# Performance work log

Measured on AMD Instinct MI355X. Metric: run time of the kernel, lower is better.

Reference implementation:

```python
import jax, jax.numpy as jnp
import numpy as np

C = 512
HEADS = 8
B, H, W = 2, 64, 64


def setup_inputs() -> dict:
    key = jax.random.key(0)
    k1, k2, k3, k4, k5 = jax.random.split(key, 5)
    s = 1.0 / np.sqrt(C)
    return {
        "hidden_states": jax.random.normal(k1, (B, C, H, W), dtype=jnp.float32),
        "qkv_w": jax.random.normal(k2, (3 * C, C), dtype=jnp.float32) * s,
        "qkv_b": jax.random.normal(k3, (3 * C,), dtype=jnp.float32) * 0.02,
        "proj_w": jax.random.normal(k4, (C, C), dtype=jnp.float32) * s,
        "proj_b": jax.random.normal(k5, (C,), dtype=jnp.float32) * 0.02,
    }


def reference(hidden_states, qkv_w, qkv_b, proj_w, proj_b):
    b, c, h, w = hidden_states.shape
    n = h * w  # sequence length
    heads = HEADS
    dim_head = c // heads
    scale = dim_head ** -0.5

    x = hidden_states.reshape(b, c, n)  # [b, c, n]
    # 1x1 conv1d == matmul over channel dim
    qkv = jnp.einsum("oc,bcn->bon", qkv_w, x) + qkv_b[None, :, None]  # [b, 3c, n]
    q, k, v = jnp.split(qkv, 3, axis=1)
    # [b, heads, dim_head, n] -> [b, heads, n, dim_head]
    def split_heads(t):
        return t.reshape(b, heads, dim_head, n).transpose(0, 1, 3, 2)
    q, k, v = split_heads(q), split_heads(k), split_heads(v)

    attn = jnp.einsum("bhqd,bhkd->bhqk", q, k) * scale  # [b, heads, n, n]
    attn = jax.nn.softmax(attn, axis=-1)
    out = jnp.einsum("bhqk,bhkd->bhqd", attn, v)  # [b, heads, n, dim_head]
    out = out.transpose(0, 1, 3, 2).reshape(b, c, n)  # [b, c, n]
    out = jnp.einsum("oc,bcn->bon", proj_w, out) + proj_b[None, :, None]
    return out  # [b, c, h*w] (matches torch module, no reshape back)
```

## Files before the change

kernel.cpp:

```cpp
#include <hip/hip_runtime.h>


#include <stdint.h>

typedef __attribute__((ext_vector_type(8))) short s16x8;
typedef __attribute__((ext_vector_type(4))) float f32x4;
typedef __attribute__((ext_vector_type(16))) float f32x16;
typedef __attribute__((ext_vector_type(4))) unsigned short u16x4;
typedef __attribute__((ext_vector_type(2))) unsigned u32x2;
typedef __attribute__((ext_vector_type(4))) unsigned u32x4;

__device__ __forceinline__ unsigned short f2bf(float f) {
  unsigned u = __builtin_bit_cast(unsigned, f);
  u += 0x7fffu + ((u >> 16) & 1u);
  return (unsigned short)(u >> 16);
}

__device__ __forceinline__ float bf2f(short s) {
  return __builtin_bit_cast(float, ((unsigned)(unsigned short)s) << 16);
}

__device__ __forceinline__ unsigned cvt_pk_bf16(float lo, float hi) {
  unsigned r;
  asm("v_cvt_pk_bf16_f32 %0, %1, %2" : "=v"(r) : "v"(lo), "v"(hi));
  return r;
}

__device__ __forceinline__ void gl_lds16(const void* g, void* l) {
  auto gp = reinterpret_cast<const __attribute__((address_space(1))) char*>(
      reinterpret_cast<uintptr_t>(g));
  auto lp = reinterpret_cast<__attribute__((address_space(3))) char*>(
      reinterpret_cast<uintptr_t>(l));
  __builtin_amdgcn_global_load_lds(gp, lp, 16, 0, 0);
}

__global__ __launch_bounds__(256) void prep_weights(
    const float* __restrict__ qkv_w, const float* __restrict__ proj_w,
    short* __restrict__ wq, short* __restrict__ wp) {
  int t = blockIdx.x * 256 + threadIdx.x;
  const int NQ = 1536 * 512 / 4;
  if (t < NQ) {
    float4 v = ((const float4*)qkv_w)[t];
    u16x4 o; o[0] = f2bf(v.x); o[1] = f2bf(v.y); o[2] = f2bf(v.z); o[3] = f2bf(v.w);
    ((u16x4*)wq)[t] = o;
  } else {
    int t2 = t - NQ;
    float4 v = ((const float4*)proj_w)[t2];
    u16x4 o; o[0] = f2bf(v.x); o[1] = f2bf(v.y); o[2] = f2bf(v.z); o[3] = f2bf(v.w);
    ((u16x4*)wp)[t2] = o;
  }
}

__global__ __launch_bounds__(256) void prep_transpose(
    const float* __restrict__ x, short* __restrict__ xt) {
  __shared__ short TL[64 * 72];
  const int b = blockIdx.z, c0 = blockIdx.y * 64, n0 = blockIdx.x * 64;
  const int t = threadIdx.x;
  const int cr = t >> 4, n4 = (t & 15) * 4;
#pragma unroll
  for (int i = 0; i < 4; i++) {
    int c = cr + i * 16;
    float4 v = *(const float4*)(x + ((size_t)(b * 512 + c0 + c)) * 4096 + n0 + n4);
    TL[(n4 + 0) * 72 + c] = (short)f2bf(v.x);
    TL[(n4 + 1) * 72 + c] = (short)f2bf(v.y);
    TL[(n4 + 2) * 72 + c] = (short)f2bf(v.z);
    TL[(n4 + 3) * 72 + c] = (short)f2bf(v.w);
  }
  __syncthreads();
  const int n = t >> 2;
#pragma unroll
  for (int s2 = 0; s2 < 2; s2++) {
    int s = (t & 3) * 2 + s2;
    s16x8 v = *(const s16x8*)&TL[n * 72 + s * 8];
    *(s16x8*)(xt + ((size_t)(b * 4096 + n0 + n)) * 512 + c0 + s * 8) = v;
  }
}

__global__ __launch_bounds__(256) void qkv_gemm(
    const short* __restrict__ wq, const short* __restrict__ xt,
    const float* __restrict__ qkv_b,
    short* __restrict__ qkbuf,
    short* __restrict__ vbuf) {
  __shared__ short Al[128 * 40];
  __shared__ short Bl[128 * 40];
  const int b = blockIdx.z;
  const int m0 = blockIdx.y * 128, n0 = blockIdx.x * 128;
  const bool swapped = (blockIdx.y < 8);
  const int t = threadIdx.x, lane = t & 63, wid = t >> 6;
  const int wr = wid >> 1, wc = wid & 1;
  const int srow = t >> 1, scol = (t & 1) * 16;
  const short* gA = wq + (size_t)(m0 + srow) * 512 + scol;
  const short* gB = xt + ((size_t)(b * 4096 + n0 + srow)) * 512 + scol;
  short* lA = &Al[srow * 40 + scol];
  short* lB = &Bl[srow * 40 + scol];
  const short* As = swapped ? Bl : Al;
  const short* Bs = swapped ? Al : Bl;
  f32x4 acc[4][4] = {};
  for (int ks = 0; ks < 16; ks++) {
    *(s16x8*)lA       = *(const s16x8*)(gA + ks * 32);
    *(s16x8*)(lA + 8) = *(const s16x8*)(gA + ks * 32 + 8);
    *(s16x8*)lB       = *(const s16x8*)(gB + ks * 32);
    *(s16x8*)(lB + 8) = *(const s16x8*)(gB + ks * 32 + 8);
    __syncthreads();
    s16x8 af[4], bf[4];
#pragma unroll
    for (int i = 0; i < 4; i++) {
      af[i] = *(const s16x8*)&As[(wr * 64 + i * 16 + (lane & 15)) * 40 + ((lane >> 4) << 3)];
      bf[i] = *(const s16x8*)&Bs[(wc * 64 + i * 16 + (lane & 15)) * 40 + ((lane >> 4) << 3)];
    }
#pragma unroll
    for (int i = 0; i < 4; i++)
#pragma unroll
      for (int j = 0; j < 4; j++)
        acc[i][j] = __builtin_amdgcn_mfma_f32_16x16x32_bf16(af[i], bf[j], acc[i][j], 0, 0, 0);
    __syncthreads();
  }
  if (!swapped) {
#pragma unroll
    for (int i = 0; i < 4; i++)
#pragma unroll
      for (int r = 0; r < 4; r++) {
        int orow = m0 + wr * 64 + i * 16 + ((lane >> 4) << 2) + r;
        float bias = qkv_b[orow];
#pragma unroll
        for (int j = 0; j < 4; j++) {
          int ncol = n0 + wc * 64 + j * 16 + (lane & 15);
          vbuf[((size_t)(b * 512 + orow - 1024)) * 4096 + ncol] = (short)f2bf(acc[i][j][r] + bias);
        }
      }
  } else {
    const float qs = (m0 < 512) ? 0.18033688f : 1.0f;
#pragma unroll
    for (int j = 0; j < 4; j++) {
      int ocol = m0 + wc * 64 + j * 16 + (lane & 15);
      float bias = qkv_b[ocol];
#pragma unroll
      for (int i = 0; i < 4; i++)
#pragma unroll
        for (int r = 0; r < 4; r++) {
          int nrow = n0 + wr * 64 + i * 16 + ((lane >> 4) << 2) + r;
          qkbuf[((size_t)(b * 4096 + nrow)) * 1024 + ocol] = (short)f2bf((acc[i][j][r] + bias) * qs);
        }
    }
  }
}

__global__ __launch_bounds__(256) void flash_attn(
    const short* __restrict__ qkbuf, const short* __restrict__ vbuf,
    short* __restrict__ opart,
    float* __restrict__ mlbuf) {
  __shared__ short Kl[2][64 * 64];
  __shared__ short Vl[2][64 * 64];
  const int t = threadIdx.x, lane = t & 63, wid = t >> 6;
  const int hi = lane >> 5, q32 = lane & 31;
  const int j = blockIdx.x;
  const int lid = ((j & 7) << 7) + (j >> 3);
  const int bh = lid >> 6, b = bh >> 3, h = bh & 7;
  const int rest = lid & 63;
  const int qc = rest >> 1, half = rest & 1;
  const int qb = qc * 128 + wid * 32;
  const int kt0 = half * 32;

  s16x8 qf[4];
  {
    const short* qrow = qkbuf + ((size_t)(b * 4096 + qb + q32)) * 1024 + h * 64 + hi * 8;
#pragma unroll
    for (int dc = 0; dc < 4; dc++) qf[dc] = *(const s16x8*)(qrow + dc * 16);
  }

  f32x16 oacc[2] = {};
  float m = -__builtin_inff();
  float l = 0.f;

  const int lrow = lane >> 3;
  const int lcolb = ((lane & 7) << 4) ^ (lrow << 4);
  const char* kp0 = (const char*)(qkbuf + ((size_t)(b * 4096 + kt0 * 64 + wid * 16 + lrow)) * 1024
                                  + 512 + h * 64) + lcolb;
  const char* kp1 = kp0 + 8 * 2048;
  const char* vp0 = (const char*)(vbuf + ((size_t)(b * 512 + h * 64 + wid * 16 + lrow)) * 4096
                                  + kt0 * 64) + lcolb;
  const char* vp1 = vp0 + 8 * 8192;

#define ISSUE_TILE(bi)                                                      \
  do {                                                                      \
    gl_lds16(kp0, &Kl[bi][(wid * 16 + 0) * 64]);                            \
    gl_lds16(kp1, &Kl[bi][(wid * 16 + 8) * 64]);                            \
    gl_lds16(vp0, &Vl[bi][(wid * 16 + 0) * 64]);                            \
    gl_lds16(vp1, &Vl[bi][(wid * 16 + 8) * 64]);                            \
    kp0 += 131072; kp1 += 131072; vp0 += 128; vp1 += 128;                   \
  } while (0)

  const int ksw = (q32 & 7) << 4;

  auto do_tile = [&](const short* Klb, const short* Vlb) {
#pragma unroll
    for (int kb = 0; kb < 2; kb++) {
      f32x16 st = {};
      const char* kr = (const char*)(Klb + (kb * 32 + q32) * 64);
      __builtin_amdgcn_s_setprio(1);
#pragma unroll
      for (int dc = 0; dc < 4; dc++) {
        s16x8 kf = *(const s16x8*)(kr + ((dc * 32 + hi * 16) ^ ksw));
        st = __builtin_amdgcn_mfma_f32_32x32x16_bf16(kf, qf[dc], st, 0, 0, 0);
      }
      __builtin_amdgcn_s_setprio(0);
      float x0 = fmaxf(st[0], st[1]),  x1 = fmaxf(st[2], st[3]);
      float x2 = fmaxf(st[4], st[5]),  x3 = fmaxf(st[6], st[7]);
      float x4 = fmaxf(st[8], st[9]),  x5 = fmaxf(st[10], st[11]);
      float x6 = fmaxf(st[12], st[13]), x7 = fmaxf(st[14], st[15]);
      x0 = fmaxf(x0, x1); x2 = fmaxf(x2, x3); x4 = fmaxf(x4, x5); x6 = fmaxf(x6, x7);
      x0 = fmaxf(x0, x2); x4 = fmaxf(x4, x6);
      float tm = fmaxf(x0, x4);
      tm = fmaxf(tm, __shfl_xor(tm, 32));
      if (!__all(tm <= m + 8.f)) {
        float mn = fmaxf(m, tm);
        float alpha = exp2f(m - mn);
        m = mn;
        l *= alpha;
#pragma unroll
        for (int di = 0; di < 2; di++)
#pragma unroll
          for (int r2 = 0; r2 < 16; r2++) oacc[di][r2] *= alpha;
      }
      float p[16];
      float ps = 0.f;
#pragma unroll
      for (int r2 = 0; r2 < 16; r2++) { p[r2] = exp2f(st[r2] - m); ps += p[r2]; }
      l += ps;
#pragma unroll
      for (int kh = 0; kh < 2; kh++) {
        unsigned A  = cvt_pk_bf16(p[kh * 8 + 0], p[kh * 8 + 1]);
        unsigned Bu = cvt_pk_bf16(p[kh * 8 + 4], p[kh * 8 + 5]);
        unsigned C  = cvt_pk_bf16(p[kh * 8 + 2], p[kh * 8 + 3]);
        unsigned D  = cvt_pk_bf16(p[kh * 8 + 6], p[kh * 8 + 7]);
        u32x2 r0 = __builtin_amdgcn_permlane32_swap(A, Bu, false, false);
        u32x2 r1 = __builtin_amdgcn_permlane32_swap(C, D, false, false);
        u32x4 uu; uu[0] = r0[0]; uu[1] = r1[0]; uu[2] = r0[1]; uu[3] = r1[1];
        s16x8 pf = __builtin_bit_cast(s16x8, uu);
        __builtin_amdgcn_s_setprio(1);
#pragma unroll
        for (int di = 0; di < 2; di++) {
          const char* vr = (const char*)(Vlb + (di * 32 + q32) * 64);
          s16x8 vf = *(const s16x8*)(vr + ((kb * 64 + kh * 32 + hi * 16) ^ ksw));
          oacc[di] = __builtin_amdgcn_mfma_f32_32x32x16_bf16(vf, pf, oacc[di], 0, 0, 0);
        }
        __builtin_amdgcn_s_setprio(0);
      }
    }
  };

  ISSUE_TILE(0);
#pragma unroll 1
  for (int it = 0; it < 16; it++) {
    __syncthreads();
    ISSUE_TILE(1);
    do_tile(Kl[0], Vl[0]);
    __syncthreads();
    if (it < 15) ISSUE_TILE(0);
    do_tile(Kl[1], Vl[1]);
  }
#undef ISSUE_TILE

  l += __shfl_xor(l, 32);
  const size_t prow = ((size_t)(half * 16 + bh) * 4096 + qb + q32) * 64;
#pragma unroll
  for (int di = 0; di < 2; di++)
#pragma unroll
    for (int blk = 0; blk < 4; blk++) {
      uint2 w;
      w.x = cvt_pk_bf16(oacc[di][blk * 4 + 0], oacc[di][blk * 4 + 1]);
      w.y = cvt_pk_bf16(oacc[di][blk * 4 + 2], oacc[di][blk * 4 + 3]);
      *(uint2*)(opart + prow + di * 32 + blk * 8 + hi * 4) = w;
    }
  if (hi == 0) {
    const size_t mrow = (size_t)(half * 16 + bh) * 4096 + qb + q32;
    ((float2*)mlbuf)[mrow] = make_float2(m, l);
  }
}

__global__ __launch_bounds__(256) void merge_halves(
    const short* __restrict__ opart, const float* __restrict__ mlbuf,
    short* __restrict__ aout) {
  const int row = blockIdx.x * 256 + threadIdx.x;
  const int bh = row >> 12, q = row & 4095, b = bh >> 3, h = bh & 7;
  float2 ml0 = ((const float2*)mlbuf)[row];
  float2 ml1 = ((const float2*)mlbuf)[65536 + row];
  float mm = fmaxf(ml0.x, ml1.x);
  float w0 = exp2f(ml0.x - mm), w1 = exp2f(ml1.x - mm);
  float inv = 1.f / (w0 * ml0.y + w1 * ml1.y);
  w0 *= inv; w1 *= inv;
  const s16x8* r0 = (const s16x8*)(opart + (size_t)row * 64);
  const s16x8* r1 = (const s16x8*)(opart + ((size_t)65536 + row) * 64);
  short* po = aout + ((size_t)(b * 4096 + q)) * 512 + h * 64;
#pragma unroll
  for (int sg = 0; sg < 8; sg++) {
    s16x8 a0 = r0[sg], a1 = r1[sg];
    float v[8];
#pragma unroll
    for (int i = 0; i < 8; i++) v[i] = w0 * bf2f(a0[i]) + w1 * bf2f(a1[i]);
    u32x4 uu;
#pragma unroll
    for (int k = 0; k < 4; k++) uu[k] = cvt_pk_bf16(v[2 * k], v[2 * k + 1]);
    *(s16x8*)(po + sg * 8) = __builtin_bit_cast(s16x8, uu);
  }
}

__global__ __launch_bounds__(256) void proj_gemm(
    const short* __restrict__ wp, const short* __restrict__ aout,
    const float* __restrict__ proj_b, float* __restrict__ out) {
  __shared__ short Al[128 * 40];
  __shared__ short Bl[128 * 40];
  const int b = blockIdx.z;
  const int m0 = blockIdx.y * 128, n0 = blockIdx.x * 128;
  const int t = threadIdx.x, lane = t & 63, wid = t >> 6;
  const int wr = wid >> 1, wc = wid & 1;
  const int srow = t >> 1, scol = (t & 1) * 16;
  const short* gA = wp + (size_t)(m0 + srow) * 512 + scol;
  const short* gB = aout + ((size_t)(b * 4096 + n0 + srow)) * 512 + scol;
  short* lA = &Al[srow * 40 + scol];
  short* lB = &Bl[srow * 40 + scol];
  f32x4 acc[4][4] = {};
  for (int ks = 0; ks < 16; ks++) {
    *(s16x8*)lA       = *(const s16x8*)(gA + ks * 32);
    *(s16x8*)(lA + 8) = *(const s16x8*)(gA + ks * 32 + 8);
    *(s16x8*)lB       = *(const s16x8*)(gB + ks * 32);
    *(s16x8*)(lB + 8) = *(const s16x8*)(gB + ks * 32 + 8);
    __syncthreads();
    s16x8 af[4], bf[4];
#pragma unroll
    for (int i = 0; i < 4; i++) {
      af[i] = *(const s16x8*)&Al[(wr * 64 + i * 16 + (lane & 15)) * 40 + ((lane >> 4) << 3)];
      bf[i] = *(const s16x8*)&Bl[(wc * 64 + i * 16 + (lane & 15)) * 40 + ((lane >> 4) << 3)];
    }
#pragma unroll
    for (int i = 0; i < 4; i++)
#pragma unroll
      for (int j = 0; j < 4; j++)
        acc[i][j] = __builtin_amdgcn_mfma_f32_16x16x32_bf16(af[i], bf[j], acc[i][j], 0, 0, 0);
    __syncthreads();
  }
#pragma unroll
  for (int i = 0; i < 4; i++)
#pragma unroll
    for (int r = 0; r < 4; r++) {
      int orow = m0 + wr * 64 + i * 16 + ((lane >> 4) << 2) + r;
      float bias = proj_b[orow];
#pragma unroll
      for (int j = 0; j < 4; j++) {
        int ncol = n0 + wc * 64 + j * 16 + (lane & 15);
        out[((size_t)(b * 512 + orow)) * 4096 + ncol] = acc[i][j][r] + bias;
      }
    }
}

extern "C" void kernel_launch(void* const* d_in, const int* in_sizes, int n_in,
                              void* d_out, int out_size, void* d_ws, size_t ws_size,
                              hipStream_t stream) {
  const float* x      = (const float*)d_in[0];
  const float* qkv_w  = (const float*)d_in[1];
  const float* qkv_b  = (const float*)d_in[2];
  const float* proj_w = (const float*)d_in[3];
  const float* proj_b = (const float*)d_in[4];
  float* out = (float*)d_out;
  char* ws = (char*)d_ws;
  short* wq = (short*)(ws);
  short* wp = (short*)(ws + 1572864);
  short* xt = (short*)(ws + 2097152);
  short* qk = (short*)(ws + 10485760);
  short* vb = (short*)(ws + 27262976);
  short* ao = (short*)(ws + 35651584);
  short* op = (short*)(ws + 44040192);
  float* ml = (float*)(ws + 60817408);

  prep_weights  <<<1024, 256, 0, stream>>>(qkv_w, proj_w, wq, wp);
  prep_transpose<<<dim3(64, 8, 2), 256, 0, stream>>>(x, xt);
  qkv_gemm      <<<dim3(32, 12, 2), 256, 0, stream>>>(wq, xt, qkv_b, qk, vb);
  flash_attn    <<<1024, 256, 0, stream>>>(qk, vb, op, ml);
  merge_halves  <<<256, 256, 0, stream>>>(op, ml, ao);
  proj_gemm     <<<dim3(32, 4, 2), 256, 0, stream>>>(wp, ao, proj_b, out);
}
```

Measured before the change: 254.9 us.

## Double-buffer QKV and proj GEMM tiles with direct global-to-LDS loads and swizzle

Both 1x1-conv GEMMs now use two LDS buffers per operand. Each buffer is filled with direct global-to-LDS loads (gl_lds16) for the next K step, issued right after the barrier so they overlap the current step's MFMAs, which removes one barrier per iteration. The padded 40-element row layout becomes an XOR-swizzled 32-element layout to avoid LDS bank conflicts without padding. MFMA sections are wrapped in s_setprio raises. The change relies on gl_lds16 being defined in the unseen part of the file and on its asynchronous completion being ordered correctly by the single barrier.

Result: faster. 240.0 us (-5.9%).

```diff
diff --git a/kernel.cpp b/kernel.cpp
--- a/kernel.cpp
+++ b/kernel.cpp
@@ -81,40 +81,57 @@
     const float* __restrict__ qkv_b,
     short* __restrict__ qkbuf,
     short* __restrict__ vbuf) {
-  __shared__ short Al[128 * 40];
-  __shared__ short Bl[128 * 40];
+  __shared__ short Al[2][128 * 32];
+  __shared__ short Bl[2][128 * 32];
   const int b = blockIdx.z;
   const int m0 = blockIdx.y * 128, n0 = blockIdx.x * 128;
   const bool swapped = (blockIdx.y < 8);
   const int t = threadIdx.x, lane = t & 63, wid = t >> 6;
   const int wr = wid >> 1, wc = wid & 1;
-  const int srow = t >> 1, scol = (t & 1) * 16;
-  const short* gA = wq + (size_t)(m0 + srow) * 512 + scol;
-  const short* gB = xt + ((size_t)(b * 4096 + n0 + srow)) * 512 + scol;
-  short* lA = &Al[srow * 40 + scol];
-  short* lB = &Bl[srow * 40 + scol];
-  const short* As = swapped ? Bl : Al;
-  const short* Bs = swapped ? Al : Bl;
+  const int rowoff = lane >> 2;
+  const int srcswz = (((lane & 3) ^ (rowoff & 3)) << 4);
+  const char* gA = (const char*)(wq + (size_t)(m0 + wid * 16 + rowoff) * 512) + srcswz;
+  const char* gB = (const char*)(xt + ((size_t)(b * 4096 + n0 + wid * 16 + rowoff)) * 512) + srcswz;
+  char* lA0 = (char*)&Al[0][0] + (wid * 16) * 64;
+  char* lA1 = (char*)&Al[1][0] + (wid * 16) * 64;
+  char* lB0 = (char*)&Bl[0][0] + (wid * 16) * 64;
+  char* lB1 = (char*)&Bl[1][0] + (wid * 16) * 64;
+
+#define GISSUE(bi, ks)                                                      \
+  do {                                                                      \
+    gl_lds16(gA + (ks) * 64,         (bi) ? lA1 : lA0);                     \
+    gl_lds16(gA + 65536 + (ks) * 64, ((bi) ? lA1 : lA0) + 64 * 64);         \
+    gl_lds16(gB + (ks) * 64,         (bi) ? lB1 : lB0);                     \
+    gl_lds16(gB + 65536 + (ks) * 64, ((bi) ? lB1 : lB0) + 64 * 64);         \
+  } while (0)
+
+  const int g4 = (lane >> 4) << 4;
+  const int rsw = (lane & 3) << 4;
   f32x4 acc[4][4] = {};
+
+  GISSUE(0, 0);
+#pragma unroll 1
   for (int ks = 0; ks < 16; ks++) {
-    *(s16x8*)lA       = *(const s16x8*)(gA + ks * 32);
-    *(s16x8*)(lA + 8) = *(const s16x8*)(gA + ks * 32 + 8);
-    *(s16x8*)lB       = *(const s16x8*)(gB + ks * 32);
-    *(s16x8*)(lB + 8) = *(const s16x8*)(gB + ks * 32 + 8);
     __syncthreads();
+    if (ks < 15) GISSUE((ks + 1) & 1, ks + 1);
+    const int bi = ks & 1;
+    const short* As = swapped ? Bl[bi] : Al[bi];
+    const short* Bs = swapped ? Al[bi] : Bl[bi];
     s16x8 af[4], bf[4];
 #pragma unroll
     for (int i = 0; i < 4; i++) {
-      af[i] = *(const s16x8*)&As[(wr * 64 + i * 16 + (lane & 15)) * 40 + ((lane >> 4) << 3)];
-      bf[i] = *(const s16x8*)&Bs[(wc * 64 + i * 16 + (lane & 15)) * 40 + ((lane >> 4) << 3)];
-    }
+      af[i] = *(const s16x8*)((const char*)As + (wr * 64 + i * 16 + (lane & 15)) * 64 + (g4 ^ rsw));
+      bf[i] = *(const s16x8*)((const char*)Bs + (wc * 64 + i * 16 + (lane & 15)) * 64 + (g4 ^ rsw));
+    }
+    __builtin_amdgcn_s_setprio(1);
 #pragma unroll
     for (int i = 0; i < 4; i++)
 #pragma unroll
       for (int j = 0; j < 4; j++)
         acc[i][j] = __builtin_amdgcn_mfma_f32_16x16x32_bf16(af[i], bf[j], acc[i][j], 0, 0, 0);
-    __syncthreads();
-  }
+    __builtin_amdgcn_s_setprio(0);
+  }
+#undef GISSUE
   if (!swapped) {
 #pragma unroll
     for (int i = 0; i < 4; i++)
@@ -308,37 +325,54 @@
 __global__ __launch_bounds__(256) void proj_gemm(
     const short* __restrict__ wp, const short* __restrict__ aout,
     const float* __restrict__ proj_b, float* __restrict__ out) {
-  __shared__ short Al[128 * 40];
-  __shared__ short Bl[128 * 40];
+  __shared__ short Al[2][128 * 32];
+  __shared__ short Bl[2][128 * 32];
   const int b = blockIdx.z;
   const int m0 = blockIdx.y * 128, n0 = blockIdx.x * 128;
   const int t = threadIdx.x, lane = t & 63, wid = t >> 6;
   const int wr = wid >> 1, wc = wid & 1;
-  const int srow = t >> 1, scol = (t & 1) * 16;
-  const short* gA = wp + (size_t)(m0 + srow) * 512 + scol;
-  const short* gB = aout + ((size_t)(b * 4096 + n0 + srow)) * 512 + scol;
-  short* lA = &Al[srow * 40 + scol];
-  short* lB = &Bl[srow * 40 + scol];
+  const int rowoff = lane >> 2;
+  const int srcswz = (((lane & 3) ^ (rowoff & 3)) << 4);
+  const char* gA = (const char*)(wp + (size_t)(m0 + wid * 16 + rowoff) * 512) + srcswz;
+  const char* gB = (const char*)(aout + ((size_t)(b * 4096 + n0 + wid * 16 + rowoff)) * 512) + srcswz;
+  char* lA0 = (char*)&Al[0][0] + (wid * 16) * 64;
+  char* lA1 = (char*)&Al[1][0] + (wid * 16) * 64;
+  char* lB0 = (char*)&Bl[0][0] + (wid * 16) * 64;
+  char* lB1 = (char*)&Bl[1][0] + (wid * 16) * 64;
+
+#define GISSUE(bi, ks)                                                      \
+  do {                                                                      \
+    gl_lds16(gA + (ks) * 64,         (bi) ? lA1 : lA0);                     \
+    gl_lds16(gA + 65536 + (ks) * 64, ((bi) ? lA1 : lA0) + 64 * 64);         \
+    gl_lds16(gB + (ks) * 64,         (bi) ? lB1 : lB0);                     \
+    gl_lds16(gB + 65536 + (ks) * 64, ((bi) ? lB1 : lB0) + 64 * 64);         \
+  } while (0)
+
+  const int g4 = (lane >> 4) << 4;
+  const int rsw = (lane & 3) << 4;
   f32x4 acc[4][4] = {};
+
+  GISSUE(0, 0);
+#pragma unroll 1
   for (int ks = 0; ks < 16; ks++) {
-    *(s16x8*)lA       = *(const s16x8*)(gA + ks * 32);
-    *(s16x8*)(lA + 8) = *(const s16x8*)(gA + ks * 32 + 8);
-    *(s16x8*)lB       = *(const s16x8*)(gB + ks * 32);
-    *(s16x8*)(lB + 8) = *(const s16x8*)(gB + ks * 32 + 8);
     __syncthreads();
+    if (ks < 15) GISSUE((ks + 1) & 1, ks + 1);
+    const int bi = ks & 1;
     s16x8 af[4], bf[4];
 #pragma unroll
     for (int i = 0; i < 4; i++) {
-      af[i] = *(const s16x8*)&Al[(wr * 64 + i * 16 + (lane & 15)) * 40 + ((lane >> 4) << 3)];
-      bf[i] = *(const s16x8*)&Bl[(wc * 64 + i * 16 + (lane & 15)) * 40 + ((lane >> 4) << 3)];
-    }
+      af[i] = *(const s16x8*)((const char*)Al[bi] + (wr * 64 + i * 16 + (lane & 15)) * 64 + (g4 ^ rsw));
+      bf[i] = *(const s16x8*)((const char*)Bl[bi] + (wc * 64 + i * 16 + (lane & 15)) * 64 + (g4 ^ rsw));
+    }
+    __builtin_amdgcn_s_setprio(1);
 #pragma unroll
     for (int i = 0; i < 4; i++)
 #pragma unroll
       for (int j = 0; j < 4; j++)
         acc[i][j] = __builtin_amdgcn_mfma_f32_16x16x32_bf16(af[i], bf[j], acc[i][j], 0, 0, 0);
-    __syncthreads();
-  }
+    __builtin_amdgcn_s_setprio(0);
+  }
+#undef GISSUE
 #pragma unroll
   for (int i = 0; i < 4; i++)
 #pragma unroll
```
